# Performance work log

Hardware: AMD Instinct MI355X
Metric: run time of the kernel (lower is better)

Reference implementation:

```python
import jax, jax.numpy as jnp
import numpy as np

B, C, H, W, D = 2, 256, 40, 40, 40
HEADS = 8


def _conv1x1(x, w, b):
    # 1x1x1 Conv3d == pointwise channel mix: x [B,C,H,W,D], w [O,C], b [O]
    return jnp.einsum('bchwd,oc->bohwd', x, w) + b[None, :, None, None, None]


def setup_inputs() -> dict:
    key = jax.random.key(0)
    ks = jax.random.split(key, 9)
    s = 1.0 / np.sqrt(C)
    return {
        'x': jax.random.normal(ks[0], (B, C, H, W, D), dtype=jnp.float32),
        'wq': jax.random.normal(ks[1], (C, C), dtype=jnp.float32) * s,
        'bq': jax.random.normal(ks[2], (C,), dtype=jnp.float32) * 0.01,
        'wk': jax.random.normal(ks[3], (C, C), dtype=jnp.float32) * s,
        'bk': jax.random.normal(ks[4], (C,), dtype=jnp.float32) * 0.01,
        'wv': jax.random.normal(ks[5], (C, C), dtype=jnp.float32) * s,
        'bv': jax.random.normal(ks[6], (C,), dtype=jnp.float32) * 0.01,
        'wp': jax.random.normal(ks[7], (C, C), dtype=jnp.float32) * s,
        'bp': jax.random.normal(ks[8], (C,), dtype=jnp.float32) * 0.01,
    }


def reference(x, wq, bq, wk, bk, wv, bv, wp, bp):
    b, ch, h, w, d = x.shape
    heads = HEADS
    hd = ch // heads
    scale = hd ** -0.5
    # q/k/v projections are identical across the three branches -> compute once
    q = _conv1x1(x, wq, bq)
    k = _conv1x1(x, wk, bk)
    v = _conv1x1(x, wv, bv)

    def branch(s1, s2, s3):
        # row-major reshape, exactly matching torch .view semantics
        qh = q.reshape(b, heads, hd, s1, s2, s3)
        kh = k.reshape(b, heads, hd, s1, s2, s3)
        vh = v.reshape(b, heads, hd, s1, s2, s3)
        # matmul over last two axes: attend along s2 with s3 as feature dim
        attn = jax.nn.softmax(qh @ jnp.swapaxes(kh, -1, -2) * scale, axis=-1)
        return (attn @ vh).reshape(b, ch, h, w, d)

    out = branch(h, w, d) + branch(w, h, d) + branch(d, h, w)
    return _conv1x1(out, wp, bp)
```

## Files before the change

### kernel.cpp

```cpp
#include <hip/hip_runtime.h>

#define NB 2
#define NC 256
#define NHH 40
#define NSP 64000
#define PL 1600
#define SCALE 0.17677669529663687f

typedef unsigned short u16;
typedef unsigned int   u32;

typedef __attribute__((ext_vector_type(8))) short bf16x8;
typedef __attribute__((ext_vector_type(4))) float f32x4;

__device__ __forceinline__ float bf2f(u16 u) {
    union { u32 i; float f; } c; c.i = ((u32)u) << 16; return c.f;
}
__device__ __forceinline__ u16 f2bf(float f) {
    union { u32 i; float f; } c; c.f = f; u32 x = c.i;
    return (u16)((x + 0x7fffu + ((x >> 16) & 1u)) >> 16);
}
__device__ __forceinline__ u32 pack2(float a, float b) {
    return (u32)f2bf(a) | ((u32)f2bf(b) << 16);
}
__device__ __forceinline__ f32x4 zero4() {
    f32x4 z; z[0] = 0.f; z[1] = 0.f; z[2] = 0.f; z[3] = 0.f; return z;
}
__device__ __forceinline__ bf16x8 zero8() {
    bf16x8 z;
#pragma unroll
    for (int e = 0; e < 8; ++e) z[e] = 0;
    return z;
}

__global__ __launch_bounds__(256, 2) void qkv_mfma(
    const float* __restrict__ x,
    const float* __restrict__ wq, const float* __restrict__ bq,
    const float* __restrict__ wk, const float* __restrict__ bk,
    const float* __restrict__ wv, const float* __restrict__ bv,
    u16* __restrict__ q, u16* __restrict__ k, u16* __restrict__ v)
{
    const int b    = blockIdx.z;
    const int n0   = blockIdx.x * 64;
    const int t    = threadIdx.x;
    const int lane = t & 63;
    const int wid  = t >> 6;
    const int o0w  = wid * 64;

    __shared__ u16 xs[64][264];
    __shared__ u16 wsm[2][256][40];

    const float* xb = x + (size_t)b * NC * NSP;

    {
        const int p  = t >> 4;
        const int nn = (t & 15) << 2;
#pragma unroll
        for (int it = 0; it < 8; ++it) {
            const int c = (it * 16 + p) * 2;
            const float4 fa = *(const float4*)(xb + (size_t)c * NSP + n0 + nn);
            const float4 fb = *(const float4*)(xb + (size_t)(c + 1) * NSP + n0 + nn);
            *(u32*)&xs[nn + 0][c] = pack2(fa.x, fb.x);
            *(u32*)&xs[nn + 1][c] = pack2(fa.y, fb.y);
            *(u32*)&xs[nn + 2][c] = pack2(fa.z, fb.z);
            *(u32*)&xs[nn + 3][c] = pack2(fa.w, fb.w);
        }
    }

    const int wo = t >> 3;
    const int wc = (t & 7) << 2;
    {
#pragma unroll
        for (int r = 0; r < 8; ++r) {
            const int o = r * 32 + wo;
            const float4 w4 = *(const float4*)(wq + (size_t)o * NC + wc);
            ushort4 pk;
            pk.x = f2bf(w4.x); pk.y = f2bf(w4.y); pk.z = f2bf(w4.z); pk.w = f2bf(w4.w);
            *(ushort4*)&wsm[0][o][wc] = pk;
        }
    }
    __syncthreads();

    f32x4 acc[4][4];
#pragma unroll
    for (int i = 0; i < 4; ++i)
#pragma unroll
        for (int j = 0; j < 4; ++j) acc[i][j] = zero4();

    const int row = lane & 15;
    const int kg  = (lane >> 4) << 3;

    int cur = 0;
    for (int step = 0; step < 24; ++step) {
        const int m  = step >> 3;
        const int kc = step & 7;
        const bool pf = (step + 1 < 24);

        float4 wreg[8];
        if (pf) {
            const int m2  = (step + 1) >> 3;
            const int kc2 = (step + 1) & 7;
            const float* wm = (m2 == 0) ? wq : ((m2 == 1) ? wk : wv);
#pragma unroll
            for (int r = 0; r < 8; ++r) {
                const int o = r * 32 + wo;
                wreg[r] = *(const float4*)(wm + (size_t)o * NC + kc2 * 32 + wc);
            }
        }

        bf16x8 af[4], bfr[4];
#pragma unroll
        for (int i = 0; i < 4; ++i)
            af[i] = *(const bf16x8*)&wsm[cur][o0w + 16 * i + row][kg];
#pragma unroll
        for (int j = 0; j < 4; ++j)
            bfr[j] = *(const bf16x8*)&xs[16 * j + row][kc * 32 + kg];
#pragma unroll
        for (int i = 0; i < 4; ++i)
#pragma unroll
            for (int j = 0; j < 4; ++j)
                acc[i][j] = __builtin_amdgcn_mfma_f32_16x16x32_bf16(
                    af[i], bfr[j], acc[i][j], 0, 0, 0);

        __syncthreads();

        if (pf) {
#pragma unroll
            for (int r = 0; r < 8; ++r) {
                const int o = r * 32 + wo;
                ushort4 pk;
                pk.x = f2bf(wreg[r].x); pk.y = f2bf(wreg[r].y);
                pk.z = f2bf(wreg[r].z); pk.w = f2bf(wreg[r].w);
                *(ushort4*)&wsm[cur ^ 1][o][wc] = pk;
            }
        }

        if (kc == 7) {
            u16* op = ((m == 0) ? q : ((m == 1) ? k : v)) + (size_t)b * NC * NSP;
            const float* bm = (m == 0) ? bq : ((m == 1) ? bk : bv);
#pragma unroll
            for (int i = 0; i < 4; ++i) {
#pragma unroll
                for (int r = 0; r < 4; ++r) {
                    const int o = o0w + 16 * i + ((lane >> 4) << 2) + r;
                    const float bb = bm[o];
#pragma unroll
                    for (int j = 0; j < 4; ++j) {
                        const int n = n0 + 16 * j + row;
                        op[(size_t)o * NSP + n] = f2bf(acc[i][j][r] + bb);
                    }
                }
            }
#pragma unroll
            for (int i = 0; i < 4; ++i)
#pragma unroll
                for (int j = 0; j < 4; ++j) acc[i][j] = zero4();
        }

        __syncthreads();
        cur ^= 1;
    }
}

__global__ __launch_bounds__(64, 4) void attn_mfma(
    const u16* __restrict__ q, const u16* __restrict__ k,
    const u16* __restrict__ v, u16* __restrict__ a)
{
    const int s = blockIdx.x;
    const size_t base = (size_t)s * PL;
    const int l = threadIdx.x & 63;
    const int g = l >> 4;
    const int c = l & 15;

    __shared__ u16 vs[48][56];
    __shared__ u16 ps[48][56];

#pragma unroll
    for (int it = 0; it < 3; ++it) {
        const int t = l + it * 64;
        *(u32*)&vs[t >> 2][40 + ((t & 3) << 1)] = 0u;
    }

#pragma unroll
    for (int it = 0; it < 7; ++it) {
        const int idx = l + it * 64;
        if (idx < 400) {
            const int j = idx / 10, d4 = (idx % 10) << 2;
            const ushort4 vv = *(const ushort4*)(v + base + j * 40 + d4);
            vs[d4 + 0][j] = vv.x; vs[d4 + 1][j] = vv.y;
            vs[d4 + 2][j] = vv.z; vs[d4 + 3][j] = vv.w;
        }
    }

    f32x4 sacc[3][3];
#pragma unroll
    for (int mt = 0; mt < 3; ++mt)
#pragma unroll
        for (int jt = 0; jt < 3; ++jt) sacc[mt][jt] = zero4();

    {
        bf16x8 aq[3], bk0[3];
#pragma unroll
        for (int mt = 0; mt < 3; ++mt)
            aq[mt] = *(const bf16x8*)(q + base + (size_t)(mt * 16 + c) * 40 + g * 8);
#pragma unroll
        for (int jt = 0; jt < 3; ++jt)
            bk0[jt] = *(const bf16x8*)(k + base + (size_t)(jt * 16 + c) * 40 + g * 8);
#pragma unroll
        for (int mt = 0; mt < 3; ++mt)
#pragma unroll
            for (int jt = 0; jt < 3; ++jt)
                sacc[mt][jt] = __builtin_amdgcn_mfma_f32_16x16x32_bf16(
                    aq[mt], bk0[jt], sacc[mt][jt], 0, 0, 0);

        bf16x8 aq1[3], bk1[3];
#pragma unroll
        for (int mt = 0; mt < 3; ++mt)
            aq1[mt] = (g == 0)
                ? *(const bf16x8*)(q + base + (size_t)(mt * 16 + c) * 40 + 32)
                : zero8();
#pragma unroll
        for (int jt = 0; jt < 3; ++jt)
            bk1[jt] = (g == 0)
                ? *(const bf16x8*)(k + base + (size_t)(jt * 16 + c) * 40 + 32)
                : zero8();
#pragma unroll
        for (int mt = 0; mt < 3; ++mt)
#pragma unroll
            for (int jt = 0; jt < 3; ++jt)
                sacc[mt][jt] = __builtin_amdgcn_mfma_f32_16x16x32_bf16(
                    aq1[mt], bk1[jt], sacc[mt][jt], 0, 0, 0);
    }

    const bool val2 = (c < 8);
#pragma unroll
    for (int mt = 0; mt < 3; ++mt) {
#pragma unroll
        for (int r = 0; r < 4; ++r) {
            const float v0 = sacc[mt][0][r];
            const float v1 = sacc[mt][1][r];
            const float v2 = sacc[mt][2][r];
            float mx = fmaxf(fmaxf(v0, v1), val2 ? v2 : -1e30f);
#pragma unroll
            for (int off = 1; off < 16; off <<= 1)
                mx = fmaxf(mx, __shfl_xor(mx, off, 64));
            const float p0 = __expf((v0 - mx) * SCALE);
            const float p1 = __expf((v1 - mx) * SCALE);
            const float p2 = val2 ? __expf((v2 - mx) * SCALE) : 0.f;
            float sum = p0 + p1 + p2;
#pragma unroll
            for (int off = 1; off < 16; off <<= 1)
                sum += __shfl_xor(sum, off, 64);
            const float inv = 3.0f / sum;
            const int ri = mt * 16 + g * 4 + r;
            ps[ri][c]      = f2bf(p0 * inv);
            ps[ri][c + 16] = f2bf(p1 * inv);
            ps[ri][c + 32] = f2bf(p2 * inv);
        }
    }
    __syncthreads();

    f32x4 oacc[3][3];
#pragma unroll
    for (int mt = 0; mt < 3; ++mt)
#pragma unroll
        for (int nt = 0; nt < 3; ++nt) oacc[mt][nt] = zero4();

    {
        bf16x8 pa[3], vb_[3];
#pragma unroll
        for (int mt = 0; mt < 3; ++mt)
            pa[mt] = *(const bf16x8*)&ps[mt * 16 + c][g * 8];
#pragma unroll
        for (int nt = 0; nt < 3; ++nt)
            vb_[nt] = *(const bf16x8*)&vs[nt * 16 + c][g * 8];
#pragma unroll
        for (int mt = 0; mt < 3; ++mt)
#pragma unroll
            for (int nt = 0; nt < 3; ++nt)
                oacc[mt][nt] = __builtin_amdgcn_mfma_f32_16x16x32_bf16(
                    pa[mt], vb_[nt], oacc[mt][nt], 0, 0, 0);

        bf16x8 pa1[3], vb1[3];
#pragma unroll
        for (int mt = 0; mt < 3; ++mt)
            pa1[mt] = (g < 2) ? *(const bf16x8*)&ps[mt * 16 + c][32 + g * 8] : zero8();
#pragma unroll
        for (int nt = 0; nt < 3; ++nt)
            vb1[nt] = (g < 2) ? *(const bf16x8*)&vs[nt * 16 + c][32 + g * 8] : zero8();
#pragma unroll
        for (int mt = 0; mt < 3; ++mt)
#pragma unroll
            for (int nt = 0; nt < 3; ++nt)
                oacc[mt][nt] = __builtin_amdgcn_mfma_f32_16x16x32_bf16(
                    pa1[mt], vb1[nt], oacc[mt][nt], 0, 0, 0);
    }
    __syncthreads();

#pragma unroll
    for (int mt = 0; mt < 3; ++mt) {
        if (mt == 2 && g >= 2) continue;
#pragma unroll
        for (int r = 0; r < 4; ++r) {
            const int ri = mt * 16 + g * 4 + r;
#pragma unroll
            for (int nt = 0; nt < 3; ++nt) {
                if (nt == 2 && c >= 8) continue;
                ps[ri][nt * 16 + c] = f2bf(oacc[mt][nt][r]);
            }
        }
    }
    __syncthreads();

#pragma unroll
    for (int it = 0; it < 7; ++it) {
        const int idx = l + it * 64;
        if (idx < 400) {
            const int i = idx / 10, d4 = (idx % 10) << 2;
            *(ushort4*)(a + base + (size_t)idx * 4) = *(const ushort4*)&ps[i][d4];
        }
    }
}

__global__ __launch_bounds__(256, 2) void proj_mfma(
    const u16* __restrict__ a, const float* __restrict__ wp,
    const float* __restrict__ bp, float* __restrict__ out)
{
    const int b    = blockIdx.z;
    const int n0   = blockIdx.x * 64;
    const int t    = threadIdx.x;
    const int lane = t & 63;
    const int wid  = t >> 6;
    const int o0w  = wid * 64;

    __shared__ u16 xs[64][264];
    __shared__ u16 wsm[2][256][40];

    const u16* ab = a + (size_t)b * NC * NSP;

    {
        const int p  = t >> 4;
        const int nn = (t & 15) << 2;
#pragma unroll
        for (int it = 0; it < 8; ++it) {
            const int c = (it * 16 + p) * 2;
            const ushort4 ua = *(const ushort4*)(ab + (size_t)c * NSP + n0 + nn);
            const ushort4 ub = *(const ushort4*)(ab + (size_t)(c + 1) * NSP + n0 + nn);
            *(u32*)&xs[nn + 0][c] = (u32)ua.x | ((u32)ub.x << 16);
            *(u32*)&xs[nn + 1][c] = (u32)ua.y | ((u32)ub.y << 16);
            *(u32*)&xs[nn + 2][c] = (u32)ua.z | ((u32)ub.z << 16);
            *(u32*)&xs[nn + 3][c] = (u32)ua.w | ((u32)ub.w << 16);
        }
    }

    const int wo = t >> 3;
    const int wc = (t & 7) << 2;
    {
#pragma unroll
        for (int r = 0; r < 8; ++r) {
            const int o = r * 32 + wo;
            const float4 w4 = *(const float4*)(wp + (size_t)o * NC + wc);
            ushort4 pk;
            pk.x = f2bf(w4.x); pk.y = f2bf(w4.y); pk.z = f2bf(w4.z); pk.w = f2bf(w4.w);
            *(ushort4*)&wsm[0][o][wc] = pk;
        }
    }
    __syncthreads();

    f32x4 acc[4][4];
#pragma unroll
    for (int i = 0; i < 4; ++i)
#pragma unroll
        for (int j = 0; j < 4; ++j) acc[i][j] = zero4();

    const int row = lane & 15;
    const int kg  = (lane >> 4) << 3;

    int cur = 0;
    for (int step = 0; step < 8; ++step) {
        const bool pf = (step + 1 < 8);
        float4 wreg[8];
        if (pf) {
            const int kc2 = step + 1;
#pragma unroll
            for (int r = 0; r < 8; ++r) {
                const int o = r * 32 + wo;
                wreg[r] = *(const float4*)(wp + (size_t)o * NC + kc2 * 32 + wc);
            }
        }

        bf16x8 af[4], bfr[4];
#pragma unroll
        for (int i = 0; i < 4; ++i)
            af[i] = *(const bf16x8*)&wsm[cur][o0w + 16 * i + row][kg];
#pragma unroll
        for (int j = 0; j < 4; ++j)
            bfr[j] = *(const bf16x8*)&xs[16 * j + row][step * 32 + kg];
#pragma unroll
        for (int i = 0; i < 4; ++i)
#pragma unroll
            for (int j = 0; j < 4; ++j)
                acc[i][j] = __builtin_amdgcn_mfma_f32_16x16x32_bf16(
                    af[i], bfr[j], acc[i][j], 0, 0, 0);

        __syncthreads();

        if (pf) {
#pragma unroll
            for (int r = 0; r < 8; ++r) {
                const int o = r * 32 + wo;
                ushort4 pk;
                pk.x = f2bf(wreg[r].x); pk.y = f2bf(wreg[r].y);
                pk.z = f2bf(wreg[r].z); pk.w = f2bf(wreg[r].w);
                *(ushort4*)&wsm[cur ^ 1][o][wc] = pk;
            }
        }
        __syncthreads();
        cur ^= 1;
    }

    float* ob = out + (size_t)b * NC * NSP;
#pragma unroll
    for (int i = 0; i < 4; ++i) {
#pragma unroll
        for (int r = 0; r < 4; ++r) {
            const int o = o0w + 16 * i + ((lane >> 4) << 2) + r;
            const float bb = bp[o];
#pragma unroll
            for (int j = 0; j < 4; ++j) {
                const int n = n0 + 16 * j + row;
                ob[(size_t)o * NSP + n] = acc[i][j][r] + bb;
            }
        }
    }
}

extern "C" void kernel_launch(void* const* d_in, const int* in_sizes, int n_in,
                              void* d_out, int out_size, void* d_ws, size_t ws_size,
                              hipStream_t stream)
{
    const float* x  = (const float*)d_in[0];
    const float* wq = (const float*)d_in[1];
    const float* bq = (const float*)d_in[2];
    const float* wk = (const float*)d_in[3];
    const float* bk = (const float*)d_in[4];
    const float* wv = (const float*)d_in[5];
    const float* bv = (const float*)d_in[6];
    const float* wp = (const float*)d_in[7];
    const float* bp = (const float*)d_in[8];
    float* out = (float*)d_out;

    const size_t QE = (size_t)NB * NC * NSP;
    u16* qb = (u16*)d_ws;
    u16* kb = qb + QE;
    u16* vb = kb + QE;
    u16* ab = vb + QE;

    qkv_mfma<<<dim3(NSP / 64, 1, NB), 256, 0, stream>>>(
        x, wq, bq, wk, bk, wv, bv, qb, kb, vb);
    attn_mfma<<<dim3(NB * NC * NHH), 64, 0, stream>>>(qb, kb, vb, ab);
    proj_mfma<<<dim3(NSP / 64, 1, NB), 256, 0, stream>>>(ab, wp, bp, out);
}
```

Baseline: 281.5 us.

## Pre-convert weights to bf16 once and remove a barrier per K-step

Adds small kernels that convert the q/k/v and projection weights to bf16 once, placing them in scratch buffers (d_out for qkv, the dead q buffer for proj). The GEMM kernels then prefetch bf16 rows directly, so each block no longer repeats the fp32 load and conversion work. The change also drops one __syncthreads per step and rotates the LDS write order of the x tile to cut bank conflicts. The cost is two extra small kernel launches. Removing the barrier between the MFMA reads of one buffer and the write of the other buffer depends on the double-buffer index being correct.

```diff
diff --git a/kernel.cpp b/kernel.cpp
--- a/kernel.cpp
+++ b/kernel.cpp
@@ -33,11 +33,35 @@
     return z;
 }
 
+__global__ __launch_bounds__(256) void wcvt3(
+    const float* __restrict__ wq, const float* __restrict__ wk,
+    const float* __restrict__ wv, u16* __restrict__ dst)
+{
+    const int g   = blockIdx.x * 256 + threadIdx.x;
+    const int mat = g >> 14;
+    const int off = (g & 16383) << 2;
+    const float* s = (mat == 0) ? wq : ((mat == 1) ? wk : wv);
+    const float4 f = *(const float4*)(s + off);
+    ushort4 p;
+    p.x = f2bf(f.x); p.y = f2bf(f.y); p.z = f2bf(f.z); p.w = f2bf(f.w);
+    *(ushort4*)(dst + (mat << 16) + off) = p;
+}
+
+__global__ __launch_bounds__(256) void wcvt1(
+    const float* __restrict__ w, u16* __restrict__ dst)
+{
+    const int g   = blockIdx.x * 256 + threadIdx.x;
+    const int off = g << 2;
+    const float4 f = *(const float4*)(w + off);
+    ushort4 p;
+    p.x = f2bf(f.x); p.y = f2bf(f.y); p.z = f2bf(f.z); p.w = f2bf(f.w);
+    *(ushort4*)(dst + off) = p;
+}
+
 __global__ __launch_bounds__(256, 2) void qkv_mfma(
-    const float* __restrict__ x,
-    const float* __restrict__ wq, const float* __restrict__ bq,
-    const float* __restrict__ wk, const float* __restrict__ bk,
-    const float* __restrict__ wv, const float* __restrict__ bv,
+    const float* __restrict__ x, const u16* __restrict__ wb,
+    const float* __restrict__ bq, const float* __restrict__ bk,
+    const float* __restrict__ bv,
     u16* __restrict__ q, u16* __restrict__ k, u16* __restrict__ v)
 {
     const int b    = blockIdx.z;
@@ -53,31 +77,29 @@
     const float* xb = x + (size_t)b * NC * NSP;
 
     {
-        const int p  = t >> 4;
-        const int nn = (t & 15) << 2;
+        const int p   = t >> 4;
+        const int nn  = (t & 15) << 2;
+        const int rot = (t >> 1) & 3;
 #pragma unroll
         for (int it = 0; it < 8; ++it) {
             const int c = (it * 16 + p) * 2;
             const float4 fa = *(const float4*)(xb + (size_t)c * NSP + n0 + nn);
             const float4 fb = *(const float4*)(xb + (size_t)(c + 1) * NSP + n0 + nn);
-            *(u32*)&xs[nn + 0][c] = pack2(fa.x, fb.x);
-            *(u32*)&xs[nn + 1][c] = pack2(fa.y, fb.y);
-            *(u32*)&xs[nn + 2][c] = pack2(fa.z, fb.z);
-            *(u32*)&xs[nn + 3][c] = pack2(fa.w, fb.w);
-        }
-    }
-
-    const int wo = t >> 3;
-    const int wc = (t & 7) << 2;
-    {
-#pragma unroll
-        for (int r = 0; r < 8; ++r) {
-            const int o = r * 32 + wo;
-            const float4 w4 = *(const float4*)(wq + (size_t)o * NC + wc);
-            ushort4 pk;
-            pk.x = f2bf(w4.x); pk.y = f2bf(w4.y); pk.z = f2bf(w4.z); pk.w = f2bf(w4.w);
-            *(ushort4*)&wsm[0][o][wc] = pk;
-        }
+            u32 pk[4] = { pack2(fa.x, fb.x), pack2(fa.y, fb.y),
+                          pack2(fa.z, fb.z), pack2(fa.w, fb.w) };
+#pragma unroll
+            for (int kk = 0; kk < 4; ++kk) {
+                const int k2 = (kk + rot) & 3;
+                *(u32*)&xs[nn + k2][c] = pk[k2];
+            }
+        }
+    }
+
+    {
+        const u16* ws0 = wb + t * NC;
+#pragma unroll
+        for (int mm = 0; mm < 4; ++mm)
+            *(bf16x8*)&wsm[0][t][mm * 8] = *(const bf16x8*)(ws0 + mm * 8);
     }
     __syncthreads();
 
@@ -96,16 +118,14 @@
         const int kc = step & 7;
         const bool pf = (step + 1 < 24);
 
-        float4 wreg[8];
+        bf16x8 wreg[4];
         if (pf) {
             const int m2  = (step + 1) >> 3;
             const int kc2 = (step + 1) & 7;
-            const float* wm = (m2 == 0) ? wq : ((m2 == 1) ? wk : wv);
-#pragma unroll
-            for (int r = 0; r < 8; ++r) {
-                const int o = r * 32 + wo;
-                wreg[r] = *(const float4*)(wm + (size_t)o * NC + kc2 * 32 + wc);
-            }
+            const u16* ws2 = wb + (m2 << 16) + t * NC + kc2 * 32;
+#pragma unroll
+            for (int mm = 0; mm < 4; ++mm)
+                wreg[mm] = *(const bf16x8*)(ws2 + mm * 8);
         }
 
         bf16x8 af[4], bfr[4];
@@ -122,17 +142,10 @@
                 acc[i][j] = __builtin_amdgcn_mfma_f32_16x16x32_bf16(
                     af[i], bfr[j], acc[i][j], 0, 0, 0);
 
-        __syncthreads();
-
         if (pf) {
 #pragma unroll
-            for (int r = 0; r < 8; ++r) {
-                const int o = r * 32 + wo;
-                ushort4 pk;
-                pk.x = f2bf(wreg[r].x); pk.y = f2bf(wreg[r].y);
-                pk.z = f2bf(wreg[r].z); pk.w = f2bf(wreg[r].w);
-                *(ushort4*)&wsm[cur ^ 1][o][wc] = pk;
-            }
+            for (int mm = 0; mm < 4; ++mm)
+                *(bf16x8*)&wsm[cur ^ 1][t][mm * 8] = wreg[mm];
         }
 
         if (kc == 7) {
@@ -157,8 +170,10 @@
                 for (int j = 0; j < 4; ++j) acc[i][j] = zero4();
         }
 
-        __syncthreads();
-        cur ^= 1;
+        if (pf) {
+            __syncthreads();
+            cur ^= 1;
+        }
     }
 }
 
@@ -323,7 +338,7 @@
 }
 
 __global__ __launch_bounds__(256, 2) void proj_mfma(
-    const u16* __restrict__ a, const float* __restrict__ wp,
+    const u16* __restrict__ a, const u16* __restrict__ wpb,
     const float* __restrict__ bp, float* __restrict__ out)
 {
     const int b    = blockIdx.z;
@@ -339,31 +354,29 @@
     const u16* ab = a + (size_t)b * NC * NSP;
 
     {
-        const int p  = t >> 4;
-        const int nn = (t & 15) << 2;
+        const int p   = t >> 4;
+        const int nn  = (t & 15) << 2;
+        const int rot = (t >> 1) & 3;
 #pragma unroll
         for (int it = 0; it < 8; ++it) {
             const int c = (it * 16 + p) * 2;
             const ushort4 ua = *(const ushort4*)(ab + (size_t)c * NSP + n0 + nn);
             const ushort4 ub = *(const ushort4*)(ab + (size_t)(c + 1) * NSP + n0 + nn);
-            *(u32*)&xs[nn + 0][c] = (u32)ua.x | ((u32)ub.x << 16);
-            *(u32*)&xs[nn + 1][c] = (u32)ua.y | ((u32)ub.y << 16);
-            *(u32*)&xs[nn + 2][c] = (u32)ua.z | ((u32)ub.z << 16);
-            *(u32*)&xs[nn + 3][c] = (u32)ua.w | ((u32)ub.w << 16);
-        }
-    }
-
-    const int wo = t >> 3;
-    const int wc = (t & 7) << 2;
-    {
-#pragma unroll
-        for (int r = 0; r < 8; ++r) {
-            const int o = r * 32 + wo;
-            const float4 w4 = *(const float4*)(wp + (size_t)o * NC + wc);
-            ushort4 pk;
-            pk.x = f2bf(w4.x); pk.y = f2bf(w4.y); pk.z = f2bf(w4.z); pk.w = f2bf(w4.w);
-            *(ushort4*)&wsm[0][o][wc] = pk;
-        }
+            u32 pk[4] = { (u32)ua.x | ((u32)ub.x << 16), (u32)ua.y | ((u32)ub.y << 16),
+                          (u32)ua.z | ((u32)ub.z << 16), (u32)ua.w | ((u32)ub.w << 16) };
+#pragma unroll
+            for (int kk = 0; kk < 4; ++kk) {
+                const int k2 = (kk + rot) & 3;
+                *(u32*)&xs[nn + k2][c] = pk[k2];
+            }
+        }
+    }
+
+    {
+        const u16* ws0 = wpb + t * NC;
+#pragma unroll
+        for (int mm = 0; mm < 4; ++mm)
+            *(bf16x8*)&wsm[0][t][mm * 8] = *(const bf16x8*)(ws0 + mm * 8);
     }
     __syncthreads();
 
@@ -379,14 +392,12 @@
     int cur = 0;
     for (int step = 0; step < 8; ++step) {
         const bool pf = (step + 1 < 8);
-        float4 wreg[8];
+        bf16x8 wreg[4];
         if (pf) {
-            const int kc2 = step + 1;
-#pragma unroll
-            for (int r = 0; r < 8; ++r) {
-                const int o = r * 32 + wo;
-                wreg[r] = *(const float4*)(wp + (size_t)o * NC + kc2 * 32 + wc);
-            }
+            const u16* ws2 = wpb + t * NC + (step + 1) * 32;
+#pragma unroll
+            for (int mm = 0; mm < 4; ++mm)
+                wreg[mm] = *(const bf16x8*)(ws2 + mm * 8);
         }
 
         bf16x8 af[4], bfr[4];
@@ -403,20 +414,13 @@
                 acc[i][j] = __builtin_amdgcn_mfma_f32_16x16x32_bf16(
                     af[i], bfr[j], acc[i][j], 0, 0, 0);
 
-        __syncthreads();
-
         if (pf) {
 #pragma unroll
-            for (int r = 0; r < 8; ++r) {
-                const int o = r * 32 + wo;
-                ushort4 pk;
-                pk.x = f2bf(wreg[r].x); pk.y = f2bf(wreg[r].y);
-                pk.z = f2bf(wreg[r].z); pk.w = f2bf(wreg[r].w);
-                *(ushort4*)&wsm[cur ^ 1][o][wc] = pk;
-            }
-        }
-        __syncthreads();
-        cur ^= 1;
+            for (int mm = 0; mm < 4; ++mm)
+                *(bf16x8*)&wsm[cur ^ 1][t][mm * 8] = wreg[mm];
+            __syncthreads();
+            cur ^= 1;
+        }
     }
 
     float* ob = out + (size_t)b * NC * NSP;
@@ -456,8 +460,13 @@
     u16* vb = kb + QE;
     u16* ab = vb + QE;
 
+    u16* wqkv = (u16*)d_out;
+    u16* wpb  = qb;
+
+    wcvt3<<<192, 256, 0, stream>>>(wq, wk, wv, wqkv);
     qkv_mfma<<<dim3(NSP / 64, 1, NB), 256, 0, stream>>>(
-        x, wq, bq, wk, bk, wv, bv, qb, kb, vb);
+        x, wqkv, bq, bk, bv, qb, kb, vb);
     attn_mfma<<<dim3(NB * NC * NHH), 64, 0, stream>>>(qb, kb, vb, ab);
-    proj_mfma<<<dim3(NSP / 64, 1, NB), 256, 0, stream>>>(ab, wp, bp, out);
-}
+    wcvt1<<<64, 256, 0, stream>>>(wp, wpb);
+    proj_mfma<<<dim3(NSP / 64, 1, NB), 256, 0, stream>>>(ab, wpb, bp, out);
+}
```

After: 290.2 us. 3.1% more time.
